# Optimization experiments

Hardware: AMD Instinct MI355X
Metric: run time of the kernel (lower is better)

Reference implementation:

```python
import jax, jax.numpy as jnp
import numpy as np

N_NODES = 100000
C = 128
E = 800000
V = 50000
NEG_SLOPE = 0.2


def gat_conv(x, edges, W, att_src, att_dst, bias, num_nodes):
    """Single-head PyG-style GATConv with self-loops added (PyG default).

    edges: [2, E] with row 0 = source j, row 1 = destination i.
    """
    loops = jnp.arange(num_nodes, dtype=edges.dtype)
    src = jnp.concatenate([edges[0], loops])  # [E+N]
    dst = jnp.concatenate([edges[1], loops])

    h = x @ W.T                               # [N, C] linear transform
    a_s = h @ att_src                         # [N] per-node src score
    a_d = h @ att_dst                         # [N] per-node dst score

    e = jax.nn.leaky_relu(a_s[src] + a_d[dst], NEG_SLOPE)  # [E+N]
    # scatter-softmax over edges grouped by destination node
    m = jax.ops.segment_max(e, dst, num_segments=num_nodes)
    ex = jnp.exp(e - m[dst])
    denom = jax.ops.segment_sum(ex, dst, num_segments=num_nodes)
    alpha = ex / (denom[dst] + 1e-16)         # [E+N]

    out = jax.ops.segment_sum(alpha[:, None] * h[src], dst, num_segments=num_nodes)
    return out + bias


def setup_inputs() -> dict:
    key = jax.random.key(0)
    ks = jax.random.split(key, 12)
    s = 1.0 / np.sqrt(C)
    return {
        "embedding": jax.random.normal(ks[0], (N_NODES, C), jnp.float32),
        "W1": jax.random.normal(ks[1], (C, C), jnp.float32) * s,
        "att_src1": jax.random.normal(ks[2], (C,), jnp.float32) * s,
        "att_dst1": jax.random.normal(ks[3], (C,), jnp.float32) * s,
        "b1": jax.random.normal(ks[4], (C,), jnp.float32) * s,
        "W2": jax.random.normal(ks[5], (C, C), jnp.float32) * s,
        "att_src2": jax.random.normal(ks[6], (C,), jnp.float32) * s,
        "att_dst2": jax.random.normal(ks[7], (C,), jnp.float32) * s,
        "b2": jax.random.normal(ks[8], (C,), jnp.float32) * s,
        "edges1": jax.random.randint(ks[9], (2, E), 0, N_NODES, jnp.int64 if jax.config.jax_enable_x64 else jnp.int32),
        "edges2": jax.random.randint(ks[10], (2, E), 0, N_NODES, jnp.int64 if jax.config.jax_enable_x64 else jnp.int32),
        "idx_mapping": jax.random.randint(ks[11], (V,), 0, N_NODES, jnp.int64 if jax.config.jax_enable_x64 else jnp.int32),
    }


def reference(embedding, W1, att_src1, att_dst1, b1, W2, att_src2, att_dst2, b2,
              edges1, edges2, idx_mapping):
    h = gat_conv(embedding, edges1, W1, att_src1, att_dst1, b1, N_NODES)
    h = gat_conv(h, edges2, W2, att_src2, att_dst2, b2, N_NODES)
    return h[idx_mapping]
```

## Files before the change

### kernel.cpp

```cpp
#include <hip/hip_runtime.h>

#define N_NODES 100000
#define C_DIM 128
#define E_EDGES 800000
#define V_OUT 50000
#define EN (E_EDGES + N_NODES)
#define M2 (2 * N_NODES)
#define EN2 (2 * EN)

#define BSHIFT 9
#define NBUCK_L ((N_NODES + 511) >> 9)
#define NBUCK2 (2 * NBUCK_L)
#define CAP 8192
#define P1_CHUNK 4096
#define P1_PER_T (P1_CHUNK / 256)
#define NCHUNK ((EN2 + P1_CHUNK - 1) / P1_CHUNK)

#define XPAD 136

typedef unsigned int uint;
typedef unsigned short ushort;
typedef __attribute__((ext_vector_type(8))) short bf16x8;
typedef __attribute__((ext_vector_type(4))) float f32x4;

static __device__ __forceinline__ ushort f2bf(float f) {
    uint u = __float_as_uint(f);
    u += 0x7fffu + ((u >> 16) & 1);
    return (ushort)(u >> 16);
}

#define PREP_WBLK (C_DIM * C_DIM / 4 / 256)
#define PREP_VBLK ((V_OUT + 255) / 256)
__global__ void prep_kernel(const float* __restrict__ W1, const float* __restrict__ W2,
                            ushort* __restrict__ W1b, ushort* __restrict__ W2b,
                            const int* __restrict__ idx, int* __restrict__ vflag)
{
    const int b = blockIdx.x;
    if (b < 2 * PREP_WBLK) {
        const float* in  = (b < PREP_WBLK) ? W1 : W2;
        ushort* outp     = (b < PREP_WBLK) ? W1b : W2b;
        int i = (b % PREP_WBLK) * 256 + threadIdx.x;
        float4 v = reinterpret_cast<const float4*>(in)[i];
        ushort4 r;
        r.x = f2bf(v.x); r.y = f2bf(v.y); r.z = f2bf(v.z); r.w = f2bf(v.w);
        reinterpret_cast<ushort4*>(outp)[i] = r;
    } else {
        int v = (b - 2 * PREP_WBLK) * 256 + threadIdx.x;
        if (v < V_OUT) vflag[idx[v]] = 1;
    }
}

template <int IN_F32>
__global__ __launch_bounds__(256) void gemm_mfma(
    const void* __restrict__ xin, const ushort* __restrict__ Wb,
    const float* __restrict__ att_s, const float* __restrict__ att_d,
    ushort* __restrict__ hb, float* __restrict__ a_s, float* __restrict__ a_d)
{
    __shared__ ushort xs[64 * XPAD];
    __shared__ ushort ws[128 * XPAD];
    const int tid = threadIdx.x;
    const int nb = blockIdx.x * 64;

    {
        const int row = tid >> 2, q = tid & 3;
        const long srow = min(nb + row, N_NODES - 1);
        ushort* dst = &xs[row * XPAD + q * 32];
        if (IN_F32) {
            const float* src = (const float*)xin + srow * 128 + q * 32;
            #pragma unroll
            for (int i = 0; i < 4; ++i) {
                float4 u = *reinterpret_cast<const float4*>(src + i * 8);
                float4 v = *reinterpret_cast<const float4*>(src + i * 8 + 4);
                uint4 pk;
                pk.x = (uint)f2bf(u.x) | ((uint)f2bf(u.y) << 16);
                pk.y = (uint)f2bf(u.z) | ((uint)f2bf(u.w) << 16);
                pk.z = (uint)f2bf(v.x) | ((uint)f2bf(v.y) << 16);
                pk.w = (uint)f2bf(v.z) | ((uint)f2bf(v.w) << 16);
                *reinterpret_cast<uint4*>(dst + i * 8) = pk;
            }
        } else {
            const ushort* src = (const ushort*)xin + srow * 128 + q * 32;
            #pragma unroll
            for (int i = 0; i < 4; ++i)
                *reinterpret_cast<uint4*>(dst + i * 8) =
                    *reinterpret_cast<const uint4*>(src + i * 8);
        }
    }
    {
        const int row = tid >> 1, half = tid & 1;
        const ushort* src = Wb + row * 128 + half * 64;
        ushort* dst = &ws[row * XPAD + half * 64];
        #pragma unroll
        for (int i = 0; i < 8; ++i)
            *reinterpret_cast<uint4*>(dst + i * 8) =
                *reinterpret_cast<const uint4*>(src + i * 8);
    }
    __syncthreads();

    const int lane = tid & 63;
    const int wv   = tid >> 6;
    const int n0   = nb + wv * 16;
    if (n0 >= N_NODES) return;
    const int m    = lane & 15;
    const int quad = lane >> 4;

    bf16x8 a[4];
    #pragma unroll
    for (int ki = 0; ki < 4; ++ki)
        a[ki] = *reinterpret_cast<const bf16x8*>(&xs[(wv * 16 + m) * XPAD + quad * 8 + ki * 32]);

    float ps[4] = {0, 0, 0, 0}, pd[4] = {0, 0, 0, 0};

    #pragma unroll
    for (int ct = 0; ct < 8; ++ct) {
        const int c = ct * 16 + m;
        f32x4 acc = {0.f, 0.f, 0.f, 0.f};
        #pragma unroll
        for (int ki = 0; ki < 4; ++ki) {
            bf16x8 b = *reinterpret_cast<const bf16x8*>(&ws[c * XPAD + quad * 8 + ki * 32]);
            acc = __builtin_amdgcn_mfma_f32_16x16x32_bf16(a[ki], b, acc, 0, 0, 0);
        }
        const float asc = att_s[c], adc = att_d[c];
        #pragma unroll
        for (int r = 0; r < 4; ++r) {
            const int node = n0 + quad * 4 + r;
            hb[(long)node * 128 + c] = f2bf(acc[r]);
            ps[r] = fmaf(acc[r], asc, ps[r]);
            pd[r] = fmaf(acc[r], adc, pd[r]);
        }
    }
    #pragma unroll
    for (int r = 0; r < 4; ++r) {
        float s = ps[r], d = pd[r];
        #pragma unroll
        for (int x = 1; x < 16; x <<= 1) { s += __shfl_xor(s, x); d += __shfl_xor(d, x); }
        if (m == 0) {
            const int node = n0 + quad * 4 + r;
            a_s[node] = s; a_d[node] = d;
        }
    }
}

__global__ __launch_bounds__(256) void partition_kernel(
    const int* __restrict__ e1, const int* __restrict__ e2,
    int* __restrict__ cursor, uint* __restrict__ slab)
{
    __shared__ int cnt[NBUCK2];
    __shared__ int basearr[NBUCK2];
    const int tid = threadIdx.x;
    for (int i = tid; i < NBUCK2; i += 256) cnt[i] = 0;
    __syncthreads();

    const int e0 = blockIdx.x * P1_CHUNK;
    uint ent[P1_PER_T];
    int  bkt[P1_PER_T];
    #pragma unroll
    for (int i = 0; i < P1_PER_T; ++i) {
        int e = e0 + i * 256 + tid;
        bkt[i] = -1;
        if (e < EN2) {
            int src, dst, lb;
            if (e < EN) {
                if (e < E_EDGES) { src = e1[e]; dst = e1[E_EDGES + e]; }
                else             { src = dst = e - E_EDGES; }
                lb = 0;
            } else {
                int f = e - EN;
                if (f < E_EDGES) { src = e2[f]; dst = e2[E_EDGES + f]; }
                else             { src = dst = f - E_EDGES; }
                lb = NBUCK_L;
            }
            bkt[i] = lb + (dst >> BSHIFT);
            ent[i] = (uint)src | ((uint)(dst & 511) << 17);
            atomicAdd(&cnt[bkt[i]], 1);
        }
    }
    __syncthreads();
    for (int b = tid; b < NBUCK2; b += 256) {
        int c = cnt[b];
        basearr[b] = (c > 0) ? atomicAdd(&cursor[b], c) : 0;
        cnt[b] = 0;
    }
    __syncthreads();
    #pragma unroll
    for (int i = 0; i < P1_PER_T; ++i) {
        if (bkt[i] >= 0) {
            int r = basearr[bkt[i]] + atomicAdd(&cnt[bkt[i]], 1);
            if (r < CAP) slab[(long)bkt[i] * CAP + r] = ent[i];
        }
    }
}

__global__ void bucket_scan(const int* __restrict__ cursor, int* __restrict__ bbase)
{
    const int lane = threadIdx.x;
    int v[7]; int s = 0;
    #pragma unroll
    for (int i = 0; i < 7; ++i) {
        int idx = lane * 7 + i;
        v[i] = (idx < NBUCK2) ? cursor[idx] : 0;
        s += v[i];
    }
    int incl = s;
    #pragma unroll
    for (int d = 1; d < 64; d <<= 1) {
        int t = __shfl_up(incl, d);
        if (lane >= d) incl += t;
    }
    int excl = incl - s;
    #pragma unroll
    for (int i = 0; i < 7; ++i) {
        int idx = lane * 7 + i;
        if (idx < NBUCK2) bbase[idx] = excl;
        excl += v[i];
    }
}

__global__ __launch_bounds__(256) void local_csr(
    const uint* __restrict__ slab, const int* __restrict__ cursor,
    const int* __restrict__ bbase, int* __restrict__ offs, uint* __restrict__ esrc)
{
    __shared__ uint ent[CAP];
    __shared__ int deg[512];
    __shared__ int excl[512];
    const int b = blockIdx.x;
    const int tid = threadIdx.x;
    const int cnt = min(cursor[b], CAP);
    const int base = bbase[b];
    const int layer = (b >= NBUCK_L);
    const int node0 = (b - layer * NBUCK_L) << BSHIFT;
    const int obase = layer * N_NODES;
    const int nodes_n = min(512, N_NODES - node0);

    for (int i = tid; i < 512; i += 256) deg[i] = 0;
    __syncthreads();
    for (int i = tid; i < cnt; i += 256) {
        uint v = slab[(long)b * CAP + i];
        ent[i] = v;
        atomicAdd(&deg[v >> 17], 1);
    }
    __syncthreads();
    if (tid < 64) {
        int v8[8]; int s = 0;
        #pragma unroll
        for (int i = 0; i < 8; ++i) { v8[i] = deg[tid * 8 + i]; s += v8[i]; }
        int incl = s;
        #pragma unroll
        for (int d = 1; d < 64; d <<= 1) {
            int t = __shfl_up(incl, d);
            if (tid >= d) incl += t;
        }
        int e = incl - s;
        #pragma unroll
        for (int i = 0; i < 8; ++i) { excl[tid * 8 + i] = e; e += v8[i]; }
    }
    __syncthreads();
    for (int i = tid; i < nodes_n; i += 256)
        offs[obase + node0 + i] = base + excl[i];
    for (int i = tid; i < 512; i += 256) deg[i] = 0;
    if (tid == 0 && node0 + 512 >= N_NODES)
        offs[obase + N_NODES] = base + cnt;
    __syncthreads();
    for (int i = tid; i < cnt; i += 256) {
        uint v = ent[i];
        int dl = v >> 17;
        int r = atomicAdd(&deg[dl], 1);
        esrc[base + excl[dl] + r] = v;
    }
}

template <int MODE>
__global__ __launch_bounds__(256) void aggregate(
    const ushort* __restrict__ hb, const float* __restrict__ a_s,
    const float* __restrict__ a_d, const float* __restrict__ bias,
    const int* __restrict__ offs, const uint* __restrict__ esrc,
    const int* __restrict__ vflag, void* __restrict__ outp, int obase)
{
    const int wave = threadIdx.x >> 6;
    const int lane = threadIdx.x & 63;
    const int slot = lane >> 4;
    const int c16  = lane & 15;
    const int node = (blockIdx.x * 4 + wave) * 4 + slot;

    int start = offs[obase + node];
    int end   = offs[obase + node + 1];
    bool active = true;
    if (MODE == 1) { active = (vflag[node] != 0); if (!active) end = start; }

    const long coff = (long)(c16 << 3);
    float acc[8] = {0, 0, 0, 0, 0, 0, 0, 0};
    float dsum = 0.0f;

    if (start < end) {
        const float ad = a_d[node];
        const int e1 = end - 1;
        uint v0 = esrc[start];
        uint v1 = esrc[min(start + 1, e1)];
        uint v2 = esrc[min(start + 2, e1)];
        float as1 = a_s[v1 & 0x1ffff];
        uint4 h0 = *reinterpret_cast<const uint4*>(hb + ((long)(v0 & 0x1ffff) << 7) + coff);
        uint4 h1 = *reinterpret_cast<const uint4*>(hb + ((long)(v1 & 0x1ffff) << 7) + coff);
        float w0;
        {
            float e = a_s[v0 & 0x1ffff] + ad;
            e = (e >= 0.0f) ? e : 0.2f * e;
            w0 = __expf(e);
        }
        for (int j = start; j < end; ++j) {
            uint  v3  = esrc[min(j + 3, e1)];
            float as2 = a_s[v2 & 0x1ffff];
            uint4 h2  = *reinterpret_cast<const uint4*>(hb + ((long)(v2 & 0x1ffff) << 7) + coff);
            float e   = as1 + ad;
            e = (e >= 0.0f) ? e : 0.2f * e;
            float w1 = __expf(e);

            dsum += w0;
            acc[0] = fmaf(w0, __uint_as_float(h0.x << 16),         acc[0]);
            acc[1] = fmaf(w0, __uint_as_float(h0.x & 0xffff0000u), acc[1]);
            acc[2] = fmaf(w0, __uint_as_float(h0.y << 16),         acc[2]);
            acc[3] = fmaf(w0, __uint_as_float(h0.y & 0xffff0000u), acc[3]);
            acc[4] = fmaf(w0, __uint_as_float(h0.z << 16),         acc[4]);
            acc[5] = fmaf(w0, __uint_as_float(h0.z & 0xffff0000u), acc[5]);
            acc[6] = fmaf(w0, __uint_as_float(h0.w << 16),         acc[6]);
            acc[7] = fmaf(w0, __uint_as_float(h0.w & 0xffff0000u), acc[7]);
            w0 = w1; h0 = h1; h1 = h2; as1 = as2; v2 = v3;
        }
    }

    if (MODE == 1 && !active) return;

    const float inv = 1.0f / (dsum + 1e-16f);
    const int c0 = c16 << 3;
    const float4 b0 = *reinterpret_cast<const float4*>(bias + c0);
    const float4 b1 = *reinterpret_cast<const float4*>(bias + c0 + 4);
    float res[8];
    res[0] = fmaf(acc[0], inv, b0.x);
    res[1] = fmaf(acc[1], inv, b0.y);
    res[2] = fmaf(acc[2], inv, b0.z);
    res[3] = fmaf(acc[3], inv, b0.w);
    res[4] = fmaf(acc[4], inv, b1.x);
    res[5] = fmaf(acc[5], inv, b1.y);
    res[6] = fmaf(acc[6], inv, b1.z);
    res[7] = fmaf(acc[7], inv, b1.w);
    if (MODE == 0) {
        uint4 pk;
        pk.x = (uint)f2bf(res[0]) | ((uint)f2bf(res[1]) << 16);
        pk.y = (uint)f2bf(res[2]) | ((uint)f2bf(res[3]) << 16);
        pk.z = (uint)f2bf(res[4]) | ((uint)f2bf(res[5]) << 16);
        pk.w = (uint)f2bf(res[6]) | ((uint)f2bf(res[7]) << 16);
        *reinterpret_cast<uint4*>((ushort*)outp + ((long)node << 7) + c0) = pk;
    } else {
        float* op = (float*)outp + ((long)node << 7) + c0;
        *reinterpret_cast<float4*>(op)     = make_float4(res[0], res[1], res[2], res[3]);
        *reinterpret_cast<float4*>(op + 4) = make_float4(res[4], res[5], res[6], res[7]);
    }
}

__global__ void gather_out(const float* __restrict__ h, const int* __restrict__ idx,
                           float* __restrict__ out)
{
    int g = blockIdx.x * 256 + threadIdx.x;
    int v = g >> 5, c4 = (g & 31) << 2;
    long src = (long)idx[v] * C_DIM + c4;
    *reinterpret_cast<float4*>(out + ((long)v * C_DIM + c4)) =
        *reinterpret_cast<const float4*>(h + src);
}

extern "C" void kernel_launch(void* const* d_in, const int* in_sizes, int n_in,
                              void* d_out, int out_size, void* d_ws, size_t ws_size,
                              hipStream_t stream)
{
    const float* emb = (const float*)d_in[0];
    const float* W1  = (const float*)d_in[1];
    const float* as1 = (const float*)d_in[2];
    const float* ad1 = (const float*)d_in[3];
    const float* b1  = (const float*)d_in[4];
    const float* W2  = (const float*)d_in[5];
    const float* as2 = (const float*)d_in[6];
    const float* ad2 = (const float*)d_in[7];
    const float* b2  = (const float*)d_in[8];
    const int* edges1 = (const int*)d_in[9];
    const int* edges2 = (const int*)d_in[10];
    const int* idxm   = (const int*)d_in[11];
    float* out = (float*)d_out;

    char* p = (char*)d_ws;
    auto alloc = [&](size_t bytes) {
        char* r = p;
        p += (bytes + 255) & ~(size_t)255;
        return r;
    };
    float*  hB   = (float*)alloc((size_t)N_NODES * C_DIM * 4);
    ushort* hb   = (ushort*)alloc((size_t)N_NODES * C_DIM * 2);
    ushort* a1o  = (ushort*)alloc((size_t)N_NODES * C_DIM * 2);
    uint*   slab = (uint*)alloc((size_t)NBUCK2 * CAP * 4);
    uint*   esrc = (uint*)alloc((size_t)EN2 * 4);
    int*    offs = (int*)alloc((size_t)(M2 + 1) * 4);
    ushort* W1b  = (ushort*)alloc((size_t)C_DIM * C_DIM * 2);
    ushort* W2b  = (ushort*)alloc((size_t)C_DIM * C_DIM * 2);
    float*  aS   = (float*)alloc((size_t)N_NODES * 4);
    float*  aD   = (float*)alloc((size_t)N_NODES * 4);
    int*  bbase  = (int*)alloc((size_t)NBUCK2 * 4);
    int*  cursor = (int*)alloc((size_t)NBUCK2 * 4);
    int*  vflag  = (int*)alloc((size_t)N_NODES * 4);

    hipMemsetAsync(cursor, 0, (size_t)((char*)vflag - (char*)cursor) + (size_t)N_NODES * 4, stream);
    prep_kernel<<<2 * PREP_WBLK + PREP_VBLK, 256, 0, stream>>>(W1, W2, W1b, W2b, idxm, vflag);

    partition_kernel<<<NCHUNK, 256, 0, stream>>>(edges1, edges2, cursor, slab);
    bucket_scan<<<1, 64, 0, stream>>>(cursor, bbase);
    local_csr<<<NBUCK2, 256, 0, stream>>>(slab, cursor, bbase, offs, esrc);

    gemm_mfma<1><<<(N_NODES + 63) / 64, 256, 0, stream>>>(emb, W1b, as1, ad1, hb, aS, aD);
    aggregate<0><<<N_NODES / 16, 256, 0, stream>>>(hb, aS, aD, b1, offs, esrc, vflag, a1o, 0);

    gemm_mfma<0><<<(N_NODES + 63) / 64, 256, 0, stream>>>(a1o, W2b, as2, ad2, hb, aS, aD);
    aggregate<1><<<N_NODES / 16, 256, 0, stream>>>(hb, aS, aD, b2, offs, esrc, vflag, hB, N_NODES);

    gather_out<<<(V_OUT * 32) / 256, 256, 0, stream>>>(hB, idxm, out);
}
```

Measured before the change: 284.1 us.

## Precompute edge weights cooperatively per block into LDS before aggregation

```diff
diff --git a/kernel.cpp b/kernel.cpp
--- a/kernel.cpp
+++ b/kernel.cpp
@@ -17,6 +17,7 @@
 #define NCHUNK ((EN2 + P1_CHUNK - 1) / P1_CHUNK)
 
 #define XPAD 136
+#define LDS_E 768
 
 typedef unsigned int uint;
 typedef unsigned short ushort;
@@ -276,58 +277,81 @@
     const int* __restrict__ offs, const uint* __restrict__ esrc,
     const int* __restrict__ vflag, void* __restrict__ outp, int obase)
 {
-    const int wave = threadIdx.x >> 6;
-    const int lane = threadIdx.x & 63;
+    __shared__ uint2 ew[LDS_E];
+    const int tid = threadIdx.x;
+    const int node0 = blockIdx.x * 16;
+    const int bnode0 = (node0 >> BSHIFT) << BSHIFT;
+    const int bstart = offs[obase + node0];
+    const int bend   = offs[obase + node0 + 16];
+    const int nE = bend - bstart;
+
+    for (int i = tid; i < min(nE, LDS_E); i += 256) {
+        uint v = esrc[bstart + i];
+        float e = a_s[v & 0x1ffff] + a_d[bnode0 + (v >> 17)];
+        e = (e >= 0.0f) ? e : 0.2f * e;
+        ew[i] = make_uint2(v, __float_as_uint(__expf(e)));
+    }
+    __syncthreads();
+
+    const int wave = tid >> 6;
+    const int lane = tid & 63;
     const int slot = lane >> 4;
     const int c16  = lane & 15;
-    const int node = (blockIdx.x * 4 + wave) * 4 + slot;
-
-    int start = offs[obase + node];
-    int end   = offs[obase + node + 1];
-    bool active = true;
-    if (MODE == 1) { active = (vflag[node] != 0); if (!active) end = start; }
-
+    const int node = node0 + wave * 4 + slot;
+    if (MODE == 1 && vflag[node] == 0) return;
+
+    const int start = offs[obase + node];
+    const int end   = offs[obase + node + 1];
     const long coff = (long)(c16 << 3);
     float acc[8] = {0, 0, 0, 0, 0, 0, 0, 0};
     float dsum = 0.0f;
 
     if (start < end) {
-        const float ad = a_d[node];
-        const int e1 = end - 1;
-        uint v0 = esrc[start];
-        uint v1 = esrc[min(start + 1, e1)];
-        uint v2 = esrc[min(start + 2, e1)];
-        float as1 = a_s[v1 & 0x1ffff];
-        uint4 h0 = *reinterpret_cast<const uint4*>(hb + ((long)(v0 & 0x1ffff) << 7) + coff);
-        uint4 h1 = *reinterpret_cast<const uint4*>(hb + ((long)(v1 & 0x1ffff) << 7) + coff);
-        float w0;
-        {
-            float e = a_s[v0 & 0x1ffff] + ad;
-            e = (e >= 0.0f) ? e : 0.2f * e;
-            w0 = __expf(e);
-        }
-        for (int j = start; j < end; ++j) {
-            uint  v3  = esrc[min(j + 3, e1)];
-            float as2 = a_s[v2 & 0x1ffff];
-            uint4 h2  = *reinterpret_cast<const uint4*>(hb + ((long)(v2 & 0x1ffff) << 7) + coff);
-            float e   = as1 + ad;
-            e = (e >= 0.0f) ? e : 0.2f * e;
-            float w1 = __expf(e);
-
-            dsum += w0;
-            acc[0] = fmaf(w0, __uint_as_float(h0.x << 16),         acc[0]);
-            acc[1] = fmaf(w0, __uint_as_float(h0.x & 0xffff0000u), acc[1]);
-            acc[2] = fmaf(w0, __uint_as_float(h0.y << 16),         acc[2]);
-            acc[3] = fmaf(w0, __uint_as_float(h0.y & 0xffff0000u), acc[3]);
-            acc[4] = fmaf(w0, __uint_as_float(h0.z << 16),         acc[4]);
-            acc[5] = fmaf(w0, __uint_as_float(h0.z & 0xffff0000u), acc[5]);
-            acc[6] = fmaf(w0, __uint_as_float(h0.w << 16),         acc[6]);
-            acc[7] = fmaf(w0, __uint_as_float(h0.w & 0xffff0000u), acc[7]);
-            w0 = w1; h0 = h1; h1 = h2; as1 = as2; v2 = v3;
-        }
-    }
-
-    if (MODE == 1 && !active) return;
+        if (nE <= LDS_E) {
+            const int jr = start - bstart, jend = end - bstart;
+            const int e1 = jend - 1;
+            uint2 p0 = ew[jr];
+            uint2 p1 = ew[min(jr + 1, e1)];
+            uint2 p2 = ew[min(jr + 2, e1)];
+            uint4 h0 = *reinterpret_cast<const uint4*>(hb + ((long)(p0.x & 0x1ffff) << 7) + coff);
+            uint4 h1 = *reinterpret_cast<const uint4*>(hb + ((long)(p1.x & 0x1ffff) << 7) + coff);
+            float w1 = __uint_as_float(p1.y);
+            float w0 = __uint_as_float(p0.y);
+            for (int j = jr; j < jend; ++j) {
+                uint2 p3 = ew[min(j + 3, e1)];
+                uint4 h2 = *reinterpret_cast<const uint4*>(hb + ((long)(p2.x & 0x1ffff) << 7) + coff);
+                float w2 = __uint_as_float(p2.y);
+                dsum += w0;
+                acc[0] = fmaf(w0, __uint_as_float(h0.x << 16),         acc[0]);
+                acc[1] = fmaf(w0, __uint_as_float(h0.x & 0xffff0000u), acc[1]);
+                acc[2] = fmaf(w0, __uint_as_float(h0.y << 16),         acc[2]);
+                acc[3] = fmaf(w0, __uint_as_float(h0.y & 0xffff0000u), acc[3]);
+                acc[4] = fmaf(w0, __uint_as_float(h0.z << 16),         acc[4]);
+                acc[5] = fmaf(w0, __uint_as_float(h0.z & 0xffff0000u), acc[5]);
+                acc[6] = fmaf(w0, __uint_as_float(h0.w << 16),         acc[6]);
+                acc[7] = fmaf(w0, __uint_as_float(h0.w & 0xffff0000u), acc[7]);
+                w0 = w1; w1 = w2; h0 = h1; h1 = h2; p2 = p3;
+            }
+        } else {
+            const float ad = a_d[node];
+            for (int j = start; j < end; ++j) {
+                uint v = esrc[j];
+                float e = a_s[v & 0x1ffff] + ad;
+                e = (e >= 0.0f) ? e : 0.2f * e;
+                float w = __expf(e);
+                uint4 h = *reinterpret_cast<const uint4*>(hb + ((long)(v & 0x1ffff) << 7) + coff);
+                dsum += w;
+                acc[0] = fmaf(w, __uint_as_float(h.x << 16),         acc[0]);
+                acc[1] = fmaf(w, __uint_as_float(h.x & 0xffff0000u), acc[1]);
+                acc[2] = fmaf(w, __uint_as_float(h.y << 16),         acc[2]);
+                acc[3] = fmaf(w, __uint_as_float(h.y & 0xffff0000u), acc[3]);
+                acc[4] = fmaf(w, __uint_as_float(h.z << 16),         acc[4]);
+                acc[5] = fmaf(w, __uint_as_float(h.z & 0xffff0000u), acc[5]);
+                acc[6] = fmaf(w, __uint_as_float(h.w << 16),         acc[6]);
+                acc[7] = fmaf(w, __uint_as_float(h.w & 0xffff0000u), acc[7]);
+            }
+        }
+    }
 
     const float inv = 1.0f / (dsum + 1e-16f);
     const int c0 = c16 << 3;
```

Measured after the change: 269.8 us. 1.05x faster.
